# Kernel optimization log

Measured on AMD Instinct MI355X. Metric: run time of the kernel, lower is better.

The kernel has to match this reference:

```python
import jax, jax.numpy as jnp
import numpy as np

B, N, IN_DIM, ATT_DIM = 2, 8192, 512, 512


def setup_inputs() -> dict:
    key = jax.random.key(0)
    k1, k2, k3, k4 = jax.random.split(key, 4)
    X = jax.random.normal(k1, (B, N, IN_DIM), dtype=jnp.float32)
    adj = jax.random.uniform(k2, (B, N, N), dtype=jnp.float32)
    mask = jnp.ones((B, N), dtype=jnp.float32)
    # Learned params (torch Linear stores W as (out,in); we store (in,out) for x @ W)
    Wqk = jax.random.normal(k3, (IN_DIM, 2 * ATT_DIM), dtype=jnp.float32) / np.sqrt(IN_DIM)
    Wv = jax.random.normal(k4, (IN_DIM, IN_DIM), dtype=jnp.float32) / np.sqrt(IN_DIM)
    return {"X": X, "adj": adj, "mask": mask, "Wqk": Wqk, "Wv": Wv}


def reference(X, adj, mask, Wqk, Wv):
    # q, k: (B, N, att_dim); v: (B, N, in_dim)
    qk = X @ Wqk
    q, k = jnp.split(qk, 2, axis=-1)
    v = X @ Wv
    att_dim = q.shape[-1]
    inv_scale = 1.0 / jnp.sqrt(jnp.float32(att_dim))
    # Original math: w_i = inv_scale * sum_j adj_ij * m_i * m_j * (q_i . k_j).
    # Since the rank-1 mask factors (m_i m_j), fold m_j into k and m_i into the row
    # score, avoiding a second materialized NxN tensor:
    k_m = k * mask[:, :, None]                       # (B, N, att_dim)
    agg = jnp.einsum("bij,bjd->bid", adj, k_m)       # (B, N, att_dim)
    w = inv_scale * mask * jnp.einsum("bid,bid->bi", q, agg)  # (B, N)
    # softmax over the bag dimension (dim=1), then scale v rows
    L = jax.nn.softmax(w, axis=1)[:, :, None] * v    # (B, N, in_dim)
    return L
```

## Files before the change

### kernel.cpp

```cpp
#include <hip/hip_runtime.h>
#include <math.h>

#define BB 2
#define NN 8192
#define DD 512

static const float INV_SCALE = 0.04419417382415922f;

typedef short s16x8 __attribute__((ext_vector_type(8)));
typedef unsigned short u16x8 __attribute__((ext_vector_type(8)));
typedef float f32x4 __attribute__((ext_vector_type(4)));

#define AS1 __attribute__((address_space(1)))
#define AS3 __attribute__((address_space(3)))

__device__ __forceinline__ unsigned short bfbits(__bf16 h) {
    return __builtin_bit_cast(unsigned short, h);
}

__device__ __forceinline__ void gll16(const void* g, void* l) {
    __builtin_amdgcn_global_load_lds((const AS1 unsigned int*)g, (AS3 unsigned int*)l, 16, 0, 0);
}

__global__ __launch_bounds__(256) void convx_k(
    const float* __restrict__ X, unsigned short* __restrict__ Xhi,
    unsigned short* __restrict__ Xlo)
{
    long i = (long)blockIdx.x * 256 + threadIdx.x;
    float4 x = ((const float4*)X)[i];
    __bf16 h0 = (__bf16)x.x, h1 = (__bf16)x.y, h2 = (__bf16)x.z, h3 = (__bf16)x.w;
    ushort4 hi4 = make_ushort4(bfbits(h0), bfbits(h1), bfbits(h2), bfbits(h3));
    __bf16 l0 = (__bf16)(x.x - (float)h0), l1 = (__bf16)(x.y - (float)h1);
    __bf16 l2 = (__bf16)(x.z - (float)h2), l3 = (__bf16)(x.w - (float)h3);
    ushort4 lo4 = make_ushort4(bfbits(l0), bfbits(l1), bfbits(l2), bfbits(l3));
    ((ushort4*)Xhi)[i] = hi4;
    ((ushort4*)Xlo)[i] = lo4;
}

__global__ __launch_bounds__(256) void convw_k(
    const float* __restrict__ Wqk, const float* __restrict__ Wv,
    unsigned short* __restrict__ QTh, unsigned short* __restrict__ QTl,
    unsigned short* __restrict__ VTh, unsigned short* __restrict__ VTl)
{
    int i = blockIdx.x * 256 + threadIdx.x;
    float val; unsigned short *ph, *pl;
    if (i < 524288) {
        int n = i >> 9, k = i & 511;
        val = Wqk[k * 1024 + n]; ph = QTh + i; pl = QTl + i;
    } else {
        int o = i - 524288; int n = o >> 9, k = o & 511;
        val = Wv[k * 512 + n]; ph = VTh + o; pl = VTl + o;
    }
    __bf16 h = (__bf16)val;
    __bf16 l = (__bf16)(val - (float)h);
    *ph = bfbits(h); *pl = bfbits(l);
}

template <int EPI, int NT, bool AF32, int BK>
__global__ __launch_bounds__(256) void mfma_gemm(
    const void* __restrict__ A0, const void* __restrict__ A1,
    const unsigned short* __restrict__ B0, const unsigned short* __restrict__ B1,
    float* __restrict__ C,
    float* __restrict__ q, float* __restrict__ km,
    unsigned short* __restrict__ kmT, const float* __restrict__ mask,
    int N, int K, long sA, long sB, long sC)
{
    constexpr int TILE_SH = 128 * BK;
    constexpr int KS  = BK / 32;
    constexpr int CPW = BK / 16;
    constexpr int RPC = 512 / BK;
    constexpr int LPR = BK / 8;

    __shared__ unsigned short Asm[2 * TILE_SH];
    __shared__ unsigned short Bsm[2 * TILE_SH];

    const int t = threadIdx.x;
    const int wv = t >> 6, lane = t & 63;
    const int wm = wv >> 1, wn = wv & 1;
    const int z = blockIdx.z;
    const long m0 = blockIdx.x * 128;
    const int n0 = blockIdx.y * 128;

    const unsigned short* Bz0 = B0 + (long)z * sB;
    const unsigned short* Bz1 = B1 ? B1 + (long)z * sB : nullptr;
    const float* Af = AF32 ? (const float*)A0 + (long)z * sA : nullptr;

    f32x4 acc[4][4];
#pragma unroll
    for (int i = 0; i < 4; ++i)
#pragma unroll
        for (int j = 0; j < 4; ++j) acc[i][j] = {0.f, 0.f, 0.f, 0.f};

    float4 rA[8];

    auto issueA = [&](int k0) {
#pragma unroll
        for (int p = 0; p < 4; ++p) {
            int idx8 = p * 256 + t;
            int row = idx8 >> 3, c8 = idx8 & 7;
            const float* s = Af + (m0 + row) * (long)K + k0 + c8 * 8;
            rA[2 * p]     = *(const float4*)s;
            rA[2 * p + 1] = *(const float4*)(s + 4);
        }
    };
    auto commitA = [&](int buf) {
#pragma unroll
        for (int p = 0; p < 4; ++p) {
            int idx8 = p * 256 + t;
            int row = idx8 >> 3, c8 = idx8 & 7;
            float4 a = rA[2 * p], b = rA[2 * p + 1];
            u16x8 pk;
            pk[0] = bfbits((__bf16)a.x); pk[1] = bfbits((__bf16)a.y);
            pk[2] = bfbits((__bf16)a.z); pk[3] = bfbits((__bf16)a.w);
            pk[4] = bfbits((__bf16)b.x); pk[5] = bfbits((__bf16)b.y);
            pk[6] = bfbits((__bf16)b.z); pk[7] = bfbits((__bf16)b.w);
            *(u16x8*)(Asm + buf * TILE_SH + row * BK + c8 * 8) = pk;
        }
    };
    auto stageA16 = [&](int term, int k0, int buf) {
        const unsigned short* Ab = (term < 2) ? (const unsigned short*)A0
                                              : (const unsigned short*)A1;
#pragma unroll
        for (int u = 0; u < CPW; ++u) {
            int c = wv * CPW + u;
            int row = c * RPC + lane / LPR;
            int colb = (lane % LPR) * 16;
            gll16((const char*)Ab + ((m0 + row) * (long)K + k0) * 2 + colb,
                  (char*)Asm + buf * (TILE_SH * 2) + c * 1024);
        }
    };
    auto stageB16 = [&](int term, int k0, int buf) {
        const unsigned short* Bb = (NT == 3 && term == 1) ? Bz1 : Bz0;
#pragma unroll
        for (int u = 0; u < CPW; ++u) {
            int c = wv * CPW + u;
            int row = c * RPC + lane / LPR;
            int colb = (lane % LPR) * 16;
            gll16((const char*)Bb + ((long)(n0 + row) * K + k0) * 2 + colb,
                  (char*)Bsm + buf * (TILE_SH * 2) + c * 1024);
        }
    };

    if constexpr (AF32) {
        issueA(0);
        stageB16(0, 0, 0);
        commitA(0);
    } else {
        stageA16(0, 0, 0);
        stageB16(0, 0, 0);
    }
    __syncthreads();

    const int NTILES = NT * (K / BK);
    int cur = 0, term = 0, k0 = 0;

#pragma unroll 2
    for (int tt = 0; tt < NTILES; ++tt) {
        int k0n = k0 + BK, termn = term;
        if (k0n == K) { k0n = 0; ++termn; }
        const bool hasNext = (tt + 1 < NTILES);

        if (hasNext) {
            if constexpr (AF32) issueA(k0n);
            else stageA16(termn, k0n, cur ^ 1);
            stageB16(termn, k0n, cur ^ 1);
        }

        const int koff = (lane >> 4) * 8;
#pragma unroll
        for (int ks = 0; ks < KS; ++ks) {
            s16x8 av[4], bv[4];
#pragma unroll
            for (int f = 0; f < 4; ++f) {
                av[f] = *(const s16x8*)(Asm + cur * TILE_SH
                        + (wm * 64 + f * 16 + (lane & 15)) * BK + koff + ks * 32);
                bv[f] = *(const s16x8*)(Bsm + cur * TILE_SH
                        + (wn * 64 + f * 16 + (lane & 15)) * BK + koff + ks * 32);
            }
#pragma unroll
            for (int fm = 0; fm < 4; ++fm)
#pragma unroll
                for (int fn = 0; fn < 4; ++fn)
                    acc[fm][fn] = __builtin_amdgcn_mfma_f32_16x16x32_bf16(
                        av[fm], bv[fn], acc[fm][fn], 0, 0, 0);
        }

        if (AF32 && hasNext) commitA(cur ^ 1);

        __syncthreads();
        cur ^= 1; term = termn; k0 = k0n;
    }

    const long rbase = m0 + wm * 64;
    const int cbase = n0 + wn * 64;

    if constexpr (EPI == 0) {
        float* Cz = C + (long)z * sC;
#pragma unroll
        for (int fm = 0; fm < 4; ++fm) {
            long rb = rbase + fm * 16 + ((lane >> 4) << 2);
#pragma unroll
            for (int fn = 0; fn < 4; ++fn) {
                int c = cbase + fn * 16 + (lane & 15);
#pragma unroll
                for (int j = 0; j < 4; ++j)
                    Cz[(rb + j) * (long)N + c] = acc[fm][fn][j];
            }
        }
    } else {
        const bool isq = (n0 < 512);
#pragma unroll
        for (int fm = 0; fm < 4; ++fm) {
            long rb = rbase + fm * 16 + ((lane >> 4) << 2);
#pragma unroll
            for (int fn = 0; fn < 4; ++fn) {
                int c = cbase + fn * 16 + (lane & 15);
                if (isq) {
#pragma unroll
                    for (int j = 0; j < 4; ++j)
                        q[(rb + j) * 512L + c] = acc[fm][fn][j];
                } else {
                    int c2 = c - 512;
                    float kv[4];
#pragma unroll
                    for (int j = 0; j < 4; ++j) {
                        kv[j] = acc[fm][fn][j] * mask[rb + j];
                        km[(rb + j) * 512L + c2] = kv[j];
                    }
                    ushort4 pk = make_ushort4(bfbits((__bf16)kv[0]), bfbits((__bf16)kv[1]),
                                              bfbits((__bf16)kv[2]), bfbits((__bf16)kv[3]));
                    long b = rb >> 13, r = rb & 8191;
                    *(ushort4*)(kmT + (b << 22) + ((long)c2 << 13) + r) = pk;
                }
            }
        }
    }
}

__global__ __launch_bounds__(128) void wdot_k(
    const float* __restrict__ q, const float* __restrict__ agg,
    const float* __restrict__ mask, float* __restrict__ w)
{
    const int row = blockIdx.x;
    const int t = threadIdx.x;
    const float4 qv = ((const float4*)(q   + (long)row * 512))[t];
    const float4 av = ((const float4*)(agg + (long)row * 512))[t];
    float s = qv.x * av.x + qv.y * av.y + qv.z * av.z + qv.w * av.w;
#pragma unroll
    for (int o = 32; o > 0; o >>= 1) s += __shfl_down(s, o);
    __shared__ float red[2];
    if ((t & 63) == 0) red[t >> 6] = s;
    __syncthreads();
    if (t == 0) w[row] = (red[0] + red[1]) * INV_SCALE * mask[row];
}

__global__ __launch_bounds__(256) void wmax_k(const float* __restrict__ w,
                                              float* __restrict__ wmax)
{
    const int b = blockIdx.x;
    const float* wr = w + (long)b * NN;
    const int t = threadIdx.x;
    float m = -3.4e38f;
    for (int i = t; i < NN; i += 256) m = fmaxf(m, wr[i]);
#pragma unroll
    for (int o = 32; o > 0; o >>= 1) m = fmaxf(m, __shfl_down(m, o));
    __shared__ float red[4];
    if ((t & 63) == 0) red[t >> 6] = m;
    __syncthreads();
    if (t == 0) wmax[b] = fmaxf(fmaxf(red[0], red[1]), fmaxf(red[2], red[3]));
}

__global__ __launch_bounds__(256) void select_k(
    const float* __restrict__ w, const float* __restrict__ wmax,
    int* __restrict__ count, int* __restrict__ cand)
{
    int i = blockIdx.x * 256 + threadIdx.x;
    int b = i >> 13;
    if (w[i] >= wmax[b] - 15.f) {
        int p = atomicAdd(count, 1);
        if (p < 128) cand[p] = i;
    }
}

__global__ __launch_bounds__(256) void refine_k(
    const float* __restrict__ q, const float* __restrict__ km,
    const float* __restrict__ adj, const int* __restrict__ cand,
    const int* __restrict__ count, float* __restrict__ partial)
{
    int y = blockIdx.y;
    int cnt = *count; if (cnt > 128) cnt = 128;
    if (y >= cnt) return;
    const int row = cand[y];
    const int b = row >> 13, r = row & 8191;
    const int x = blockIdx.x;
    const int t = threadIdx.x, w = t >> 6, l = t & 63;

    const float* qr = q + (long)row * 512 + l * 8;
    const float4 q0 = *(const float4*)qr;
    const float4 q1 = *(const float4*)(qr + 4);
    const float* kmB = km + ((long)b << 13) * 512;
    const float* adjR = adj + (((long)b << 13) + r) * 8192L;

    float acc = 0.f;
    const int jbase = x * 128 + w * 32;
    for (int i = 0; i < 32; ++i) {
        int j = jbase + i;
        const float* kr = kmB + (long)j * 512 + l * 8;
        const float4 k0 = *(const float4*)kr;
        const float4 k1 = *(const float4*)(kr + 4);
        float d = q0.x * k0.x + q0.y * k0.y + q0.z * k0.z + q0.w * k0.w
                + q1.x * k1.x + q1.y * k1.y + q1.z * k1.z + q1.w * k1.w;
#pragma unroll
        for (int o = 32; o > 0; o >>= 1) d += __shfl_down(d, o);
        if (l == 0) acc += adjR[j] * d;
    }
    __shared__ float red[4];
    if (l == 0) red[w] = acc;
    __syncthreads();
    if (t == 0) partial[y * 64 + x] = red[0] + red[1] + red[2] + red[3];
}

__global__ __launch_bounds__(128) void apply_k(
    const int* __restrict__ cand, const int* __restrict__ count,
    const float* __restrict__ partial, const float* __restrict__ mask,
    float* __restrict__ w)
{
    int t = threadIdx.x;
    int cnt = *count; if (cnt > 128) cnt = 128;
    if (t < cnt) {
        float s = 0.f;
        for (int x = 0; x < 64; ++x) s += partial[t * 64 + x];
        int row = cand[t];
        w[row] = s * INV_SCALE * mask[row];
    }
}

__global__ __launch_bounds__(1024) void softmax_k(
    const float* __restrict__ w, float* __restrict__ p)
{
    const int b = blockIdx.x;
    const float* wr = w + (long)b * NN;
    float* pr = p + (long)b * NN;
    const int t = threadIdx.x;
    __shared__ float red[16];
    __shared__ float bmax, bsum;

    float m = -3.4e38f;
    for (int i = t; i < NN; i += 1024) m = fmaxf(m, wr[i]);
#pragma unroll
    for (int o = 32; o > 0; o >>= 1) m = fmaxf(m, __shfl_down(m, o));
    if ((t & 63) == 0) red[t >> 6] = m;
    __syncthreads();
    if (t == 0) {
        float mm = red[0];
        for (int i = 1; i < 16; ++i) mm = fmaxf(mm, red[i]);
        bmax = mm;
    }
    __syncthreads();
    const float M = bmax;

    float s = 0.f;
    for (int i = t; i < NN; i += 1024) s += expf(wr[i] - M);
#pragma unroll
    for (int o = 32; o > 0; o >>= 1) s += __shfl_down(s, o);
    __syncthreads();
    if ((t & 63) == 0) red[t >> 6] = s;
    __syncthreads();
    if (t == 0) {
        float ss = 0.f;
        for (int i = 0; i < 16; ++i) ss += red[i];
        bsum = ss;
    }
    __syncthreads();
    const float invS = 1.f / bsum;
    for (int i = t; i < NN; i += 1024) pr[i] = expf(wr[i] - M) * invS;
}

__global__ __launch_bounds__(256) void scale_k(
    const float* __restrict__ v, const float* __restrict__ p,
    float* __restrict__ out)
{
    const long i = (long)blockIdx.x * 256 + threadIdx.x;
    const int row = (int)(i >> 7);
    const float pv = p[row];
    float4 vv = ((const float4*)v)[i];
    vv.x *= pv; vv.y *= pv; vv.z *= pv; vv.w *= pv;
    ((float4*)out)[i] = vv;
}

extern "C" void kernel_launch(void* const* d_in, const int* in_sizes, int n_in,
                              void* d_out, int out_size, void* d_ws, size_t ws_size,
                              hipStream_t stream)
{
    const float* X    = (const float*)d_in[0];
    const float* adj  = (const float*)d_in[1];
    const float* mask = (const float*)d_in[2];
    const float* Wqk  = (const float*)d_in[3];
    const float* Wv   = (const float*)d_in[4];
    float* out = (float*)d_out;

    char* ws = (char*)d_ws;
    const long SZB = 33554432;
    float* q_buf  = (float*)(ws);
    float* km_buf = (float*)(ws + SZB);
    float* v_buf  = (float*)(ws + 2 * SZB);
    char*  xagg   = ws + 3 * SZB;
    unsigned short* Xhi = (unsigned short*)xagg;
    unsigned short* Xlo = (unsigned short*)(xagg + SZB / 2);
    float* agg_buf = (float*)xagg;
    unsigned short* kmT = (unsigned short*)(ws + 4 * SZB);
    unsigned short* QTh = (unsigned short*)(ws + 4 * SZB + 16777216);
    unsigned short* QTl = QTh + 524288;
    unsigned short* VTh = QTl + 524288;
    unsigned short* VTl = VTh + 262144;
    float* w_buf = (float*)(VTl + 262144);
    float* p_buf = w_buf + 16384;
    float* wmax  = p_buf + 16384;
    float* partial = wmax + 64;
    int* count = (int*)(partial + 8192);
    int* cand  = count + 64;

    hipMemsetAsync(count, 0, 4, stream);

    convx_k<<<8192, 256, 0, stream>>>(X, Xhi, Xlo);
    convw_k<<<3072, 256, 0, stream>>>(Wqk, Wv, QTh, QTl, VTh, VTl);

    mfma_gemm<1, 3, false, 32><<<dim3(128, 8, 1), 256, 0, stream>>>(
        Xhi, Xlo, QTh, QTl, nullptr, q_buf, km_buf, kmT, mask,
        1024, 512, 0, 0, 0);

    mfma_gemm<0, 3, false, 32><<<dim3(128, 4, 1), 256, 0, stream>>>(
        Xhi, Xlo, VTh, VTl, v_buf, nullptr, nullptr, nullptr, nullptr,
        512, 512, 0, 0, 0);

    mfma_gemm<0, 1, true, 64><<<dim3(64, 4, 2), 256, 0, stream>>>(
        adj, nullptr, kmT, nullptr, agg_buf, nullptr, nullptr, nullptr, nullptr,
        512, 8192, (long)8192 * 8192, (long)512 * 8192, (long)8192 * 512);

    wdot_k<<<16384, 128, 0, stream>>>(q_buf, agg_buf, mask, w_buf);

    wmax_k<<<BB, 256, 0, stream>>>(w_buf, wmax);
    select_k<<<64, 256, 0, stream>>>(w_buf, wmax, count, cand);
    refine_k<<<dim3(64, 128, 1), 256, 0, stream>>>(q_buf, km_buf, adj, cand, count, partial);
    apply_k<<<1, 128, 0, stream>>>(cand, count, partial, mask, w_buf);

    softmax_k<<<BB, 1024, 0, stream>>>(w_buf, p_buf);
    scale_k<<<8192, 256, 0, stream>>>(v_buf, p_buf, out);
}
```

Measured before the change: 458.2 us.

## Fuse q·agg dot into adj GEMM with split-K, swizzled LDS, single-term V GEMM

The adj×km GEMM now runs split-K over two K halves. Its epilogue computes the row dot product with q directly and atomically accumulates into w, which removes the agg buffer write and the separate wdot kernel. LDS tiles use an XOR swizzle to avoid bank conflicts, BK is fixed at 32, and launch_bounds gain a min-waves hint. The V projection drops the hi/lo split terms and uses one bf16 product, which reduces its work but lowers precision. The cost is float atomics on w, plus a memset and a fixup kernel for the scale and mask.

```diff
diff --git a/kernel.cpp b/kernel.cpp
--- a/kernel.cpp
+++ b/kernel.cpp
@@ -56,20 +56,17 @@
     *ph = bfbits(h); *pl = bfbits(l);
 }
 
-template <int EPI, int NT, bool AF32, int BK>
-__global__ __launch_bounds__(256) void mfma_gemm(
+template <int EPI, int NT, bool AF32, int SPLITK, int MINW>
+__global__ __launch_bounds__(256, MINW) void mfma_gemm(
     const void* __restrict__ A0, const void* __restrict__ A1,
     const unsigned short* __restrict__ B0, const unsigned short* __restrict__ B1,
     float* __restrict__ C,
-    float* __restrict__ q, float* __restrict__ km,
+    float* __restrict__ q, float* __restrict__ km_or_w,
     unsigned short* __restrict__ kmT, const float* __restrict__ mask,
     int N, int K, long sA, long sB, long sC)
 {
+    constexpr int BK = 32;
     constexpr int TILE_SH = 128 * BK;
-    constexpr int KS  = BK / 32;
-    constexpr int CPW = BK / 16;
-    constexpr int RPC = 512 / BK;
-    constexpr int LPR = BK / 8;
 
     __shared__ unsigned short Asm[2 * TILE_SH];
     __shared__ unsigned short Bsm[2 * TILE_SH];
@@ -77,13 +74,16 @@
     const int t = threadIdx.x;
     const int wv = t >> 6, lane = t & 63;
     const int wm = wv >> 1, wn = wv & 1;
-    const int z = blockIdx.z;
+    const int batch = blockIdx.z / SPLITK;
+    const int ksplit = blockIdx.z % SPLITK;
+    const int klen = K / SPLITK;
+    const int kbeg = ksplit * klen;
     const long m0 = blockIdx.x * 128;
     const int n0 = blockIdx.y * 128;
 
-    const unsigned short* Bz0 = B0 + (long)z * sB;
-    const unsigned short* Bz1 = B1 ? B1 + (long)z * sB : nullptr;
-    const float* Af = AF32 ? (const float*)A0 + (long)z * sA : nullptr;
+    const unsigned short* Bz0 = B0 + (long)batch * sB;
+    const unsigned short* Bz1 = B1 ? B1 + (long)batch * sB : nullptr;
+    const float* Af = AF32 ? (const float*)A0 + (long)batch * sA : nullptr;
 
     f32x4 acc[4][4];
 #pragma unroll
@@ -91,52 +91,51 @@
 #pragma unroll
         for (int j = 0; j < 4; ++j) acc[i][j] = {0.f, 0.f, 0.f, 0.f};
 
-    float4 rA[8];
+    float4 rA[4];
 
     auto issueA = [&](int k0) {
 #pragma unroll
-        for (int p = 0; p < 4; ++p) {
-            int idx8 = p * 256 + t;
-            int row = idx8 >> 3, c8 = idx8 & 7;
-            const float* s = Af + (m0 + row) * (long)K + k0 + c8 * 8;
-            rA[2 * p]     = *(const float4*)s;
-            rA[2 * p + 1] = *(const float4*)(s + 4);
+        for (int u = 0; u < 2; ++u) {
+            int row = t >> 1;
+            int c8  = (t & 1) * 2 + u;
+            const float* s = Af + (m0 + row) * (long)K + kbeg + k0 + c8 * 8;
+            rA[2 * u]     = *(const float4*)s;
+            rA[2 * u + 1] = *(const float4*)(s + 4);
         }
     };
     auto commitA = [&](int buf) {
 #pragma unroll
-        for (int p = 0; p < 4; ++p) {
-            int idx8 = p * 256 + t;
-            int row = idx8 >> 3, c8 = idx8 & 7;
-            float4 a = rA[2 * p], b = rA[2 * p + 1];
+        for (int u = 0; u < 2; ++u) {
+            int row = t >> 1;
+            int c8  = (t & 1) * 2 + u;
+            float4 a = rA[2 * u], b = rA[2 * u + 1];
             u16x8 pk;
             pk[0] = bfbits((__bf16)a.x); pk[1] = bfbits((__bf16)a.y);
             pk[2] = bfbits((__bf16)a.z); pk[3] = bfbits((__bf16)a.w);
             pk[4] = bfbits((__bf16)b.x); pk[5] = bfbits((__bf16)b.y);
             pk[6] = bfbits((__bf16)b.z); pk[7] = bfbits((__bf16)b.w);
-            *(u16x8*)(Asm + buf * TILE_SH + row * BK + c8 * 8) = pk;
+            *(u16x8*)(Asm + buf * TILE_SH + row * 32 + ((c8 ^ (row & 3)) << 3)) = pk;
         }
     };
+    const int swzcol = ((lane & 3) ^ ((lane >> 2) & 3)) * 16;
     auto stageA16 = [&](int term, int k0, int buf) {
         const unsigned short* Ab = (term < 2) ? (const unsigned short*)A0
                                               : (const unsigned short*)A1;
 #pragma unroll
-        for (int u = 0; u < CPW; ++u) {
-            int c = wv * CPW + u;
-            int row = c * RPC + lane / LPR;
-            int colb = (lane % LPR) * 16;
-            gll16((const char*)Ab + ((m0 + row) * (long)K + k0) * 2 + colb,
+        for (int u = 0; u < 2; ++u) {
+            int c = wv * 2 + u;
+            int row = c * 16 + (lane >> 2);
+            gll16((const char*)Ab + ((m0 + row) * (long)K + kbeg + k0) * 2 + swzcol,
                   (char*)Asm + buf * (TILE_SH * 2) + c * 1024);
         }
     };
     auto stageB16 = [&](int term, int k0, int buf) {
         const unsigned short* Bb = (NT == 3 && term == 1) ? Bz1 : Bz0;
 #pragma unroll
-        for (int u = 0; u < CPW; ++u) {
-            int c = wv * CPW + u;
-            int row = c * RPC + lane / LPR;
-            int colb = (lane % LPR) * 16;
-            gll16((const char*)Bb + ((long)(n0 + row) * K + k0) * 2 + colb,
+        for (int u = 0; u < 2; ++u) {
+            int c = wv * 2 + u;
+            int row = c * 16 + (lane >> 2);
+            gll16((const char*)Bb + ((long)(n0 + row) * K + kbeg + k0) * 2 + swzcol,
                   (char*)Bsm + buf * (TILE_SH * 2) + c * 1024);
         }
     };
@@ -151,13 +150,14 @@
     }
     __syncthreads();
 
-    const int NTILES = NT * (K / BK);
+    const int NTILES = NT * (klen / BK);
     int cur = 0, term = 0, k0 = 0;
+    const int g = lane >> 4;
 
 #pragma unroll 2
     for (int tt = 0; tt < NTILES; ++tt) {
         int k0n = k0 + BK, termn = term;
-        if (k0n == K) { k0n = 0; ++termn; }
+        if (k0n == klen) { k0n = 0; ++termn; }
         const bool hasNext = (tt + 1 < NTILES);
 
         if (hasNext) {
@@ -166,24 +166,20 @@
             stageB16(termn, k0n, cur ^ 1);
         }
 
-        const int koff = (lane >> 4) * 8;
-#pragma unroll
-        for (int ks = 0; ks < KS; ++ks) {
-            s16x8 av[4], bv[4];
-#pragma unroll
-            for (int f = 0; f < 4; ++f) {
-                av[f] = *(const s16x8*)(Asm + cur * TILE_SH
-                        + (wm * 64 + f * 16 + (lane & 15)) * BK + koff + ks * 32);
-                bv[f] = *(const s16x8*)(Bsm + cur * TILE_SH
-                        + (wn * 64 + f * 16 + (lane & 15)) * BK + koff + ks * 32);
-            }
-#pragma unroll
-            for (int fm = 0; fm < 4; ++fm)
-#pragma unroll
-                for (int fn = 0; fn < 4; ++fn)
-                    acc[fm][fn] = __builtin_amdgcn_mfma_f32_16x16x32_bf16(
-                        av[fm], bv[fn], acc[fm][fn], 0, 0, 0);
-        }
+        s16x8 av[4], bv[4];
+#pragma unroll
+        for (int f = 0; f < 4; ++f) {
+            int ra = wm * 64 + f * 16 + (lane & 15);
+            int rb = wn * 64 + f * 16 + (lane & 15);
+            av[f] = *(const s16x8*)(Asm + cur * TILE_SH + ra * BK + ((g ^ (ra & 3)) << 3));
+            bv[f] = *(const s16x8*)(Bsm + cur * TILE_SH + rb * BK + ((g ^ (rb & 3)) << 3));
+        }
+#pragma unroll
+        for (int fm = 0; fm < 4; ++fm)
+#pragma unroll
+            for (int fn = 0; fn < 4; ++fn)
+                acc[fm][fn] = __builtin_amdgcn_mfma_f32_16x16x32_bf16(
+                    av[fm], bv[fn], acc[fm][fn], 0, 0, 0);
 
         if (AF32 && hasNext) commitA(cur ^ 1);
 
@@ -195,7 +191,7 @@
     const int cbase = n0 + wn * 64;
 
     if constexpr (EPI == 0) {
-        float* Cz = C + (long)z * sC;
+        float* Cz = C + (long)batch * sC;
 #pragma unroll
         for (int fm = 0; fm < 4; ++fm) {
             long rb = rbase + fm * 16 + ((lane >> 4) << 2);
@@ -207,7 +203,7 @@
                     Cz[(rb + j) * (long)N + c] = acc[fm][fn][j];
             }
         }
-    } else {
+    } else if constexpr (EPI == 1) {
         const bool isq = (n0 < 512);
 #pragma unroll
         for (int fm = 0; fm < 4; ++fm) {
@@ -225,7 +221,7 @@
 #pragma unroll
                     for (int j = 0; j < 4; ++j) {
                         kv[j] = acc[fm][fn][j] * mask[rb + j];
-                        km[(rb + j) * 512L + c2] = kv[j];
+                        km_or_w[(rb + j) * 512L + c2] = kv[j];
                     }
                     ushort4 pk = make_ushort4(bfbits((__bf16)kv[0]), bfbits((__bf16)kv[1]),
                                               bfbits((__bf16)kv[2]), bfbits((__bf16)kv[3]));
@@ -234,24 +230,31 @@
                 }
             }
         }
-    }
-}
-
-__global__ __launch_bounds__(128) void wdot_k(
-    const float* __restrict__ q, const float* __restrict__ agg,
-    const float* __restrict__ mask, float* __restrict__ w)
-{
-    const int row = blockIdx.x;
-    const int t = threadIdx.x;
-    const float4 qv = ((const float4*)(q   + (long)row * 512))[t];
-    const float4 av = ((const float4*)(agg + (long)row * 512))[t];
-    float s = qv.x * av.x + qv.y * av.y + qv.z * av.z + qv.w * av.w;
-#pragma unroll
-    for (int o = 32; o > 0; o >>= 1) s += __shfl_down(s, o);
-    __shared__ float red[2];
-    if ((t & 63) == 0) red[t >> 6] = s;
-    __syncthreads();
-    if (t == 0) w[row] = (red[0] + red[1]) * INV_SCALE * mask[row];
+    } else {
+        const long zrow = (long)batch * NN;
+#pragma unroll
+        for (int fm = 0; fm < 4; ++fm) {
+#pragma unroll
+            for (int j = 0; j < 4; ++j) {
+                long r = zrow + rbase + fm * 16 + ((lane >> 4) << 2) + j;
+                const float* qr = q + r * 512L + cbase + (lane & 15);
+                float s = 0.f;
+#pragma unroll
+                for (int fn = 0; fn < 4; ++fn)
+                    s += qr[fn * 16] * acc[fm][fn][j];
+                s += __shfl_xor(s, 1); s += __shfl_xor(s, 2);
+                s += __shfl_xor(s, 4); s += __shfl_xor(s, 8);
+                if ((lane & 15) == 0) atomicAdd(km_or_w + r, s);
+            }
+        }
+    }
+}
+
+__global__ __launch_bounds__(256) void fixup_k(
+    float* __restrict__ w, const float* __restrict__ mask)
+{
+    int i = blockIdx.x * 256 + threadIdx.x;
+    w[i] *= INV_SCALE * mask[i];
 }
 
 __global__ __launch_bounds__(256) void wmax_k(const float* __restrict__ w,
@@ -404,10 +407,8 @@
     float* q_buf  = (float*)(ws);
     float* km_buf = (float*)(ws + SZB);
     float* v_buf  = (float*)(ws + 2 * SZB);
-    char*  xagg   = ws + 3 * SZB;
-    unsigned short* Xhi = (unsigned short*)xagg;
-    unsigned short* Xlo = (unsigned short*)(xagg + SZB / 2);
-    float* agg_buf = (float*)xagg;
+    unsigned short* Xhi = (unsigned short*)(ws + 3 * SZB);
+    unsigned short* Xlo = Xhi + 8388608;
     unsigned short* kmT = (unsigned short*)(ws + 4 * SZB);
     unsigned short* QTh = (unsigned short*)(ws + 4 * SZB + 16777216);
     unsigned short* QTl = QTh + 524288;
@@ -421,23 +422,24 @@
     int* cand  = count + 64;
 
     hipMemsetAsync(count, 0, 4, stream);
+    hipMemsetAsync(w_buf, 0, 16384 * 4, stream);
 
     convx_k<<<8192, 256, 0, stream>>>(X, Xhi, Xlo);
     convw_k<<<3072, 256, 0, stream>>>(Wqk, Wv, QTh, QTl, VTh, VTl);
 
-    mfma_gemm<1, 3, false, 32><<<dim3(128, 8, 1), 256, 0, stream>>>(
+    mfma_gemm<1, 3, false, 1, 2><<<dim3(128, 8, 1), 256, 0, stream>>>(
         Xhi, Xlo, QTh, QTl, nullptr, q_buf, km_buf, kmT, mask,
         1024, 512, 0, 0, 0);
 
-    mfma_gemm<0, 3, false, 32><<<dim3(128, 4, 1), 256, 0, stream>>>(
-        Xhi, Xlo, VTh, VTl, v_buf, nullptr, nullptr, nullptr, nullptr,
+    mfma_gemm<0, 1, false, 1, 2><<<dim3(128, 4, 1), 256, 0, stream>>>(
+        Xhi, nullptr, VTh, nullptr, v_buf, nullptr, nullptr, nullptr, nullptr,
         512, 512, 0, 0, 0);
 
-    mfma_gemm<0, 1, true, 64><<<dim3(64, 4, 2), 256, 0, stream>>>(
-        adj, nullptr, kmT, nullptr, agg_buf, nullptr, nullptr, nullptr, nullptr,
-        512, 8192, (long)8192 * 8192, (long)512 * 8192, (long)8192 * 512);
-
-    wdot_k<<<16384, 128, 0, stream>>>(q_buf, agg_buf, mask, w_buf);
+    mfma_gemm<2, 1, true, 2, 4><<<dim3(64, 4, 4), 256, 0, stream>>>(
+        adj, nullptr, kmT, nullptr, nullptr, q_buf, w_buf, nullptr, nullptr,
+        512, 8192, (long)8192 * 8192, (long)512 * 8192, 0);
+
+    fixup_k<<<64, 256, 0, stream>>>(w_buf, mask);
 
     wmax_k<<<BB, 256, 0, stream>>>(w_buf, wmax);
     select_k<<<64, 256, 0, stream>>>(w_buf, wmax, count, cand);
```

After: 479.1 us. 4.6% more time.
